# Kernel optimization log

Measured on AMD Instinct MI355X. Metric: run time of the kernel, lower is better.

The kernel has to match this reference:

```python
import jax, jax.numpy as jnp
import numpy as np

N, E, D, L = 50000, 800000, 128, 3  # nodes, edges, feature dim, num GraphConv layers


def setup_inputs() -> dict:
    key = jax.random.key(0)
    ks = jax.random.split(key, 6)
    x = jax.random.normal(ks[0], (N, D), dtype=jnp.float32)
    edge_index = jax.random.randint(ks[1], (2, E), 0, N, dtype=jnp.int64)
    edge_weight = jax.random.uniform(ks[2], (E,), dtype=jnp.float32)
    s = 1.0 / np.sqrt(D)  # PyG Linear default (kaiming-ish uniform bound)
    W_rel = jax.random.uniform(ks[3], (L, D, D), dtype=jnp.float32, minval=-s, maxval=s)
    b_rel = jax.random.uniform(ks[4], (L, D), dtype=jnp.float32, minval=-s, maxval=s)
    W_root = jax.random.uniform(ks[5], (L, D, D), dtype=jnp.float32, minval=-s, maxval=s)
    return {"x": x, "edge_index": edge_index, "edge_weight": edge_weight,
            "W_rel": W_rel, "b_rel": b_rel, "W_root": W_root}


def reference(x, edge_index, edge_weight, W_rel, b_rel, W_root):
    # PyG GraphConv: out = lin_rel(sum_{j->i} e_ji * x_j) + lin_root(x_i)
    src, dst = edge_index[0], edge_index[1]

    def conv(h, i):
        msg = h[src] * edge_weight[:, None]                     # [E, D] gather + per-edge scale
        agg = jax.ops.segment_sum(msg, dst, num_segments=N)     # [N, D] scatter-add
        return agg @ W_rel[i] + b_rel[i] + h @ W_root[i]

    h = x
    for i in range(L - 1):
        h = jax.nn.relu(conv(h, i))  # dropout is identity at inference
    return conv(h, L - 1)
```

## Files before the change

### kernel.cpp

```cpp
#include <hip/hip_runtime.h>

#define D 128
#define SC_IT 8

typedef __attribute__((ext_vector_type(8))) short bf16x8;
typedef __attribute__((ext_vector_type(4))) float f32x4;

__device__ __forceinline__ float uif(unsigned u) { return __uint_as_float(u); }
__device__ __forceinline__ unsigned short f2bf(float f) {
    unsigned u = __float_as_uint(f);
    u += 0x7fffu + ((u >> 16) & 1u);
    return (unsigned short)(u >> 16);
}
__device__ __forceinline__ float bf2f(unsigned short h) {
    return __uint_as_float(((unsigned)h) << 16);
}

__global__ __launch_bounds__(256) void rank_kernel(
    const int* __restrict__ dst, int* __restrict__ counts,
    int* __restrict__ rank, int E)
{
    int e = blockIdx.x * 256 + threadIdx.x;
    if (e < E) rank[e] = atomicAdd(&counts[dst[e]], 1);
}

__global__ __launch_bounds__(256) void blocksum_kernel(
    const int* __restrict__ counts, int* __restrict__ bsums, int N)
{
    __shared__ int red[256];
    int t = threadIdx.x;
    int i = blockIdx.x * 256 + t;
    red[t] = (i < N) ? counts[i] : 0;
    __syncthreads();
    #pragma unroll
    for (int off = 128; off > 0; off >>= 1) {
        if (t < off) red[t] += red[t + off];
        __syncthreads();
    }
    if (t == 0) bsums[blockIdx.x] = red[0];
}

__global__ __launch_bounds__(256) void scansums_kernel(
    int* __restrict__ bsums, int nb)
{
    __shared__ int s[256];
    int t = threadIdx.x;
    int v = (t < nb) ? bsums[t] : 0;
    s[t] = v;
    __syncthreads();
    #pragma unroll
    for (int off = 1; off < 256; off <<= 1) {
        int tmp = (t >= off) ? s[t - off] : 0;
        __syncthreads();
        s[t] += tmp;
        __syncthreads();
    }
    if (t < nb) bsums[t] = s[t] - v;
}

__global__ __launch_bounds__(256) void emit_kernel(
    const int* __restrict__ counts, const int* __restrict__ bsums,
    int* __restrict__ row_ptr, int N, int E)
{
    __shared__ int s[256];
    int t = threadIdx.x;
    int i = blockIdx.x * 256 + t;
    int v = (i < N) ? counts[i] : 0;
    s[t] = v;
    __syncthreads();
    #pragma unroll
    for (int off = 1; off < 256; off <<= 1) {
        int tmp = (t >= off) ? s[t - off] : 0;
        __syncthreads();
        s[t] += tmp;
        __syncthreads();
    }
    int excl = s[t] - v + bsums[blockIdx.x];
    if (i < N) row_ptr[i] = excl;
    if (blockIdx.x == 0 && t == 0) row_ptr[N] = E;
}

__global__ __launch_bounds__(256) void scatter_xcd_kernel(
    const int* __restrict__ src, const int* __restrict__ dst,
    const float* __restrict__ ew, const int* __restrict__ row_ptr,
    const int* __restrict__ rank, unsigned* __restrict__ edata, int E, int N)
{
    int xcd   = blockIdx.x & 7;
    int chunk = blockIdx.x >> 3;
    int lo = (int)(((long long)xcd * N) >> 3);
    int hi = (int)(((long long)(xcd + 1) * N) >> 3);
    int base = chunk * (256 * SC_IT) + threadIdx.x;
    #pragma unroll
    for (int it = 0; it < SC_IT; ++it) {
        int e = base + it * 256;
        if (e < E) {
            int d = __builtin_nontemporal_load(&dst[e]);
            if (d >= lo && d < hi) {
                int pos = row_ptr[d] + rank[e];
                unsigned pk = (unsigned)(unsigned short)
                                  __builtin_nontemporal_load(&src[e])
                            | ((unsigned)f2bf(
                                  __builtin_nontemporal_load(&ew[e])) << 16);
                edata[pos] = pk;
            }
        }
    }
}

__global__ __launch_bounds__(256) void convert_x_kernel(
    const float* __restrict__ x, short* __restrict__ Ah, int N)
{
    int t = blockIdx.x * 256 + threadIdx.x;
    if (t >= N * 64) return;
    int row = t >> 6;
    int c2  = (t & 63) * 2;
    float2 v = *(const float2*)(x + (size_t)row * D + c2);
    *(unsigned*)(Ah + (size_t)row * D + c2) =
        ((unsigned)f2bf(v.y) << 16) | f2bf(v.x);
}

__global__ __launch_bounds__(256) void convert_w_kernel(
    const float* __restrict__ Wrel, const float* __restrict__ Wroot,
    short* __restrict__ WT, int total)
{
    int t = blockIdx.x * 256 + threadIdx.x;
    if (t >= total) return;
    int l = t >> 15;
    int rem = t & 32767;
    int k = rem >> 7;
    int c = rem & 127;
    float f = (k < 128) ? Wrel[(size_t)l * 16384 + k * D + c]
                        : Wroot[(size_t)l * 16384 + (k - 128) * D + c];
    WT[(size_t)l * 32768 + c * 256 + k] = (short)f2bf(f);
}

__global__ __launch_bounds__(256) void gather_bf16(
    const short* __restrict__ Ah, short* __restrict__ aggHi,
    const unsigned* __restrict__ edata, const int* __restrict__ row_ptr, int N)
{
    int wave = (blockIdx.x * 256 + threadIdx.x) >> 6;
    int lane = threadIdx.x & 63;
    if (wave >= N) return;
    int g   = lane >> 4;
    int l16 = lane & 15;
    int beg = row_ptr[wave];
    int cnt = row_ptr[wave + 1] - beg;

    const short* hbase = Ah + l16 * 8;

    float acc[8];
    #pragma unroll
    for (int c = 0; c < 8; ++c) acc[c] = 0.f;

    for (int base = 0; base < cnt; base += 64) {
        int k = base + lane;
        int ed = 0;
        if (k < cnt) ed = (int)edata[beg + k];
        int m = min(64, cnt - base);
        for (int j = 0; j < m; j += 16) {
            int eA = __shfl(ed, j + g);
            int eB = __shfl(ed, j + 4 + g);
            int eC = __shfl(ed, j + 8 + g);
            int eD = __shfl(ed, j + 12 + g);
            float wA = uif((unsigned)eA & 0xffff0000u);
            float wB = uif((unsigned)eB & 0xffff0000u);
            float wC = uif((unsigned)eC & 0xffff0000u);
            float wD = uif((unsigned)eD & 0xffff0000u);
            bf16x8 rA = *(const bf16x8*)(hbase + (size_t)(eA & 0xffff) * D);
            bf16x8 rB = *(const bf16x8*)(hbase + (size_t)(eB & 0xffff) * D);
            bf16x8 rC = *(const bf16x8*)(hbase + (size_t)(eC & 0xffff) * D);
            bf16x8 rD = *(const bf16x8*)(hbase + (size_t)(eD & 0xffff) * D);
            #pragma unroll
            for (int c = 0; c < 8; ++c)
                acc[c] = fmaf(wA, bf2f((unsigned short)rA[c]), acc[c]);
            #pragma unroll
            for (int c = 0; c < 8; ++c)
                acc[c] = fmaf(wB, bf2f((unsigned short)rB[c]), acc[c]);
            #pragma unroll
            for (int c = 0; c < 8; ++c)
                acc[c] = fmaf(wC, bf2f((unsigned short)rC[c]), acc[c]);
            #pragma unroll
            for (int c = 0; c < 8; ++c)
                acc[c] = fmaf(wD, bf2f((unsigned short)rD[c]), acc[c]);
        }
    }

    #pragma unroll
    for (int c = 0; c < 8; ++c) {
        acc[c] += __shfl_xor(acc[c], 16);
        acc[c] += __shfl_xor(acc[c], 32);
    }

    if (g == 0) {
        bf16x8 pk;
        #pragma unroll
        for (int c = 0; c < 8; ++c) pk[c] = (short)f2bf(acc[c]);
        *(bf16x8*)(aggHi + (size_t)wave * D + l16 * 8) = pk;
    }
}

#define STAGE_W(WSRC)                                                           \
    _Pragma("unroll")                                                           \
    for (int r = 0; r < 16; ++r) {                                              \
        int u = r * 256 + tid;                                                  \
        bf16x8 v = *(const bf16x8*)((WSRC) + (size_t)u * 8);                    \
        int scol = u >> 5, sku = u & 31;                                        \
        *(bf16x8*)((char*)bsh + scol * 512 + ((sku ^ (scol & 7)) << 4)) = v;    \
    }

#define MFMA_SEG(APTR, KUOFF)                                                   \
    _Pragma("unroll")                                                           \
    for (int ks = 0; ks < 4; ++ks) {                                            \
        bf16x8 av[4];                                                           \
        _Pragma("unroll")                                                       \
        for (int m = 0; m < 4; ++m)                                             \
            av[m] = *(const bf16x8*)((APTR) + abase + (size_t)m * 16 * D        \
                                     + ks * 32 + l4 * 8);                       \
        _Pragma("unroll")                                                       \
        for (int n = 0; n < 4; ++n) {                                           \
            int col = wc * 64 + n * 16 + l15;                                   \
            int ku = (KUOFF) + ks * 4 + l4;                                     \
            bf16x8 b = *(const bf16x8*)((const char*)bsh + col * 512            \
                                        + ((ku ^ (col & 7)) << 4));             \
            _Pragma("unroll")                                                   \
            for (int m = 0; m < 4; ++m)                                         \
                acc[m][n] = __builtin_amdgcn_mfma_f32_16x16x32_bf16(            \
                    av[m], b, acc[m][n], 0, 0, 0);                              \
        }                                                                       \
    }

__global__ __launch_bounds__(256, 2) void gemm_mfma(
    const short* __restrict__ aggHi,
    const short* __restrict__ Ah, short* __restrict__ AhN,
    const short* __restrict__ WT,
    const float* __restrict__ bias, float* __restrict__ outf,
    int N, int relu, int writef)
{
    __shared__ short bsh[32768];
    int tid = threadIdx.x;
    int lane = tid & 63;
    int wid = tid >> 6;
    int wr = wid >> 1, wc = wid & 1;
    int l15 = lane & 15, l4 = lane >> 4;
    int row0 = blockIdx.x * 128;

    size_t abase = (size_t)(row0 + wr * 64 + l15) * D;

    f32x4 acc[4][4];
    #pragma unroll
    for (int m = 0; m < 4; ++m)
        #pragma unroll
        for (int n = 0; n < 4; ++n)
            acc[m][n] = (f32x4){0.f, 0.f, 0.f, 0.f};

    STAGE_W(WT);
    __syncthreads();
    MFMA_SEG(aggHi, 0);
    MFMA_SEG(Ah, 16);

    #pragma unroll
    for (int n = 0; n < 4; ++n) {
        int col = wc * 64 + n * 16 + l15;
        float bv = bias[col];
        #pragma unroll
        for (int m = 0; m < 4; ++m) {
            #pragma unroll
            for (int r = 0; r < 4; ++r) {
                int row = row0 + wr * 64 + m * 16 + l4 * 4 + r;
                if (row < N) {
                    float v = acc[m][n][r] + bv;
                    if (relu) v = fmaxf(v, 0.f);
                    if (writef) outf[(size_t)row * D + col] = v;
                    else        AhN[(size_t)row * D + col] = (short)f2bf(v);
                }
            }
        }
    }
}

extern "C" void kernel_launch(void* const* d_in, const int* in_sizes, int n_in,
                              void* d_out, int out_size, void* d_ws, size_t ws_size,
                              hipStream_t stream)
{
    const float* x     = (const float*)d_in[0];
    const int*   ei    = (const int*)d_in[1];
    const float* ew    = (const float*)d_in[2];
    const float* Wrel  = (const float*)d_in[3];
    const float* brel  = (const float*)d_in[4];
    const float* Wroot = (const float*)d_in[5];
    float* out = (float*)d_out;

    int N = in_sizes[0] / D;
    int E = in_sizes[2];
    int L = in_sizes[3] / (D * D);
    int Npad = ((N + 127) / 128) * 128;
    const int* src = ei;
    const int* dst = ei + E;
    int nb = (N + 255) / 256;

    short* Ah0   = (short*)d_ws;
    short* Ah1   = Ah0 + (size_t)Npad * D;
    short* aggHi = Ah1 + (size_t)Npad * D;
    short* WT    = aggHi + (size_t)Npad * D;
    unsigned* edata = (unsigned*)(WT + (size_t)L * 32768);
    int*   row_ptr = (int*)(edata + E);
    int*   rank    = row_ptr + (N + 1);
    int*   counts  = rank + E;
    int*   bsums   = counts + N;

    dim3 blk256(256);
    dim3 grdE((E + 255) / 256);
    dim3 grdN(nb);
    int nchunks = (E + 256 * SC_IT - 1) / (256 * SC_IT);
    dim3 grdScat(nchunks * 8);
    dim3 grdGather((N * 64 + 255) / 256);
    dim3 grdGemm(Npad / 128);
    dim3 grdCX((N * 64 + 255) / 256);
    dim3 grdCW((L * 32768 + 255) / 256);

    hipMemsetAsync(counts, 0, (size_t)N * sizeof(int), stream);
    rank_kernel<<<grdE, blk256, 0, stream>>>(dst, counts, rank, E);
    blocksum_kernel<<<grdN, blk256, 0, stream>>>(counts, bsums, N);
    scansums_kernel<<<1, blk256, 0, stream>>>(bsums, nb);
    emit_kernel<<<grdN, blk256, 0, stream>>>(counts, bsums, row_ptr, N, E);
    scatter_xcd_kernel<<<grdScat, blk256, 0, stream>>>(src, dst, ew, row_ptr,
                                                       rank, edata, E, N);

    convert_w_kernel<<<grdCW, blk256, 0, stream>>>(Wrel, Wroot, WT, L * 32768);
    convert_x_kernel<<<grdCX, blk256, 0, stream>>>(x, Ah0, N);

    for (int l = 0; l < L; ++l) {
        const short* Ain  = (l & 1) ? Ah1 : Ah0;
        short*       Aout = (l & 1) ? Ah0 : Ah1;
        gather_bf16<<<grdGather, blk256, 0, stream>>>(Ain, aggHi, edata, row_ptr, N);
        gemm_mfma<<<grdGemm, blk256, 0, stream>>>(
            aggHi, Ain, Aout, WT + (size_t)l * 32768,
            brel + (size_t)l * D, out, N, (l < L - 1) ? 1 : 0, (l == L - 1) ? 1 : 0);
    }
}
```

Baseline: 237.7 us.

## Gather neighbor features from an FP8 copy and partition rank atomics by XCD

Keeps a second FP8 (e4m3) copy of the node features next to the bf16 copy, written by convert_x and by the GEMM epilogue. The gather kernel reads that copy and decodes it with hardware cvt_pk_f32_fp8 when available, halving the bytes fetched per random neighbor row. The rank atomics are also split by destination range across XCD-mapped blocks, matching the existing scatter kernel. The trade is lower precision in the aggregated messages, extra byte-wise stores in the GEMM epilogue, and rank_kernel now reading dst eight times over.

New measurement: 243.6 us. +2.5%, slower.

```diff
diff --git a/kernel.cpp b/kernel.cpp
--- a/kernel.cpp
+++ b/kernel.cpp
@@ -5,6 +5,7 @@
 
 typedef __attribute__((ext_vector_type(8))) short bf16x8;
 typedef __attribute__((ext_vector_type(4))) float f32x4;
+typedef __attribute__((ext_vector_type(2))) unsigned uint2v;
 
 __device__ __forceinline__ float uif(unsigned u) { return __uint_as_float(u); }
 __device__ __forceinline__ unsigned short f2bf(float f) {
@@ -16,12 +17,68 @@
     return __uint_as_float(((unsigned)h) << 16);
 }
 
-__global__ __launch_bounds__(256) void rank_kernel(
+__device__ __forceinline__ unsigned char f2fp8(float f) {
+    unsigned s = (__float_as_uint(f) >> 24) & 0x80u;
+    float a = fminf(fabsf(f), 448.f);
+    unsigned b = __float_as_uint(a);
+    int e = (int)((b >> 23) & 255) - 127;
+    unsigned r;
+    if (e >= -6) {
+        unsigned rb = b + 0x7ffffu + ((b >> 20) & 1u);
+        int e8 = (int)((rb >> 23) & 255) - 120;
+        unsigned m3 = (rb >> 20) & 7u;
+        if (e8 > 15) { e8 = 15; m3 = 6; }
+        r = ((unsigned)e8 << 3) | m3;
+    } else {
+        int ni = (int)(a * 512.f + 0.5f);
+        r = (ni > 7) ? 8u : (unsigned)ni;
+    }
+    return (unsigned char)(s | r);
+}
+
+#if __has_builtin(__builtin_amdgcn_cvt_pk_f32_fp8)
+#define DECODE8(Q, F)                                                           \
+    do {                                                                        \
+        auto p0 = __builtin_amdgcn_cvt_pk_f32_fp8((Q).x, false);                \
+        auto p1 = __builtin_amdgcn_cvt_pk_f32_fp8((Q).x, true);                 \
+        auto p2 = __builtin_amdgcn_cvt_pk_f32_fp8((Q).y, false);                \
+        auto p3 = __builtin_amdgcn_cvt_pk_f32_fp8((Q).y, true);                 \
+        F[0] = p0[0]; F[1] = p0[1]; F[2] = p1[0]; F[3] = p1[1];                 \
+        F[4] = p2[0]; F[5] = p2[1]; F[6] = p3[0]; F[7] = p3[1];                 \
+    } while (0)
+#else
+__device__ __forceinline__ float fp82f_sw(unsigned b) {
+    unsigned e = (b >> 3) & 15u, m = b & 7u;
+    float v = e ? uif(((e + 120u) << 23) | (m << 20)) : (float)m * 0x1p-9f;
+    return (b & 0x80u) ? -v : v;
+}
+#define DECODE8(Q, F)                                                           \
+    do {                                                                        \
+        unsigned q0 = (Q).x, q1 = (Q).y;                                        \
+        F[0] = fp82f_sw(q0 & 255); F[1] = fp82f_sw((q0 >> 8) & 255);            \
+        F[2] = fp82f_sw((q0 >> 16) & 255); F[3] = fp82f_sw(q0 >> 24);           \
+        F[4] = fp82f_sw(q1 & 255); F[5] = fp82f_sw((q1 >> 8) & 255);            \
+        F[6] = fp82f_sw((q1 >> 16) & 255); F[7] = fp82f_sw(q1 >> 24);           \
+    } while (0)
+#endif
+
+__global__ __launch_bounds__(256) void rank_xcd_kernel(
     const int* __restrict__ dst, int* __restrict__ counts,
-    int* __restrict__ rank, int E)
-{
-    int e = blockIdx.x * 256 + threadIdx.x;
-    if (e < E) rank[e] = atomicAdd(&counts[dst[e]], 1);
+    int* __restrict__ rank, int E, int N)
+{
+    int xcd   = blockIdx.x & 7;
+    int chunk = blockIdx.x >> 3;
+    int lo = (int)(((long long)xcd * N) >> 3);
+    int hi = (int)(((long long)(xcd + 1) * N) >> 3);
+    int base = chunk * (256 * SC_IT) + threadIdx.x;
+    #pragma unroll
+    for (int it = 0; it < SC_IT; ++it) {
+        int e = base + it * 256;
+        if (e < E) {
+            int d = __builtin_nontemporal_load(&dst[e]);
+            if (d >= lo && d < hi) rank[e] = atomicAdd(&counts[d], 1);
+        }
+    }
 }
 
 __global__ __launch_bounds__(256) void blocksum_kernel(
@@ -108,7 +165,8 @@
 }
 
 __global__ __launch_bounds__(256) void convert_x_kernel(
-    const float* __restrict__ x, short* __restrict__ Ah, int N)
+    const float* __restrict__ x, short* __restrict__ Ah,
+    unsigned char* __restrict__ Ah8, int N)
 {
     int t = blockIdx.x * 256 + threadIdx.x;
     if (t >= N * 64) return;
@@ -117,6 +175,9 @@
     float2 v = *(const float2*)(x + (size_t)row * D + c2);
     *(unsigned*)(Ah + (size_t)row * D + c2) =
         ((unsigned)f2bf(v.y) << 16) | f2bf(v.x);
+    unsigned short p8 = (unsigned short)f2fp8(v.x)
+                      | ((unsigned short)f2fp8(v.y) << 8);
+    *(unsigned short*)(Ah8 + (size_t)row * D + c2) = p8;
 }
 
 __global__ __launch_bounds__(256) void convert_w_kernel(
@@ -134,8 +195,8 @@
     WT[(size_t)l * 32768 + c * 256 + k] = (short)f2bf(f);
 }
 
-__global__ __launch_bounds__(256) void gather_bf16(
-    const short* __restrict__ Ah, short* __restrict__ aggHi,
+__global__ __launch_bounds__(256) void gather_fp8(
+    const unsigned char* __restrict__ Ah8, short* __restrict__ aggHi,
     const unsigned* __restrict__ edata, const int* __restrict__ row_ptr, int N)
 {
     int wave = (blockIdx.x * 256 + threadIdx.x) >> 6;
@@ -146,7 +207,7 @@
     int beg = row_ptr[wave];
     int cnt = row_ptr[wave + 1] - beg;
 
-    const short* hbase = Ah + l16 * 8;
+    const unsigned char* hbase = Ah8 + l16 * 8;
 
     float acc[8];
     #pragma unroll
@@ -166,22 +227,23 @@
             float wB = uif((unsigned)eB & 0xffff0000u);
             float wC = uif((unsigned)eC & 0xffff0000u);
             float wD = uif((unsigned)eD & 0xffff0000u);
-            bf16x8 rA = *(const bf16x8*)(hbase + (size_t)(eA & 0xffff) * D);
-            bf16x8 rB = *(const bf16x8*)(hbase + (size_t)(eB & 0xffff) * D);
-            bf16x8 rC = *(const bf16x8*)(hbase + (size_t)(eC & 0xffff) * D);
-            bf16x8 rD = *(const bf16x8*)(hbase + (size_t)(eD & 0xffff) * D);
+            uint2v qA = *(const uint2v*)(hbase + (size_t)(eA & 0xffff) * D);
+            uint2v qB = *(const uint2v*)(hbase + (size_t)(eB & 0xffff) * D);
+            uint2v qC = *(const uint2v*)(hbase + (size_t)(eC & 0xffff) * D);
+            uint2v qD = *(const uint2v*)(hbase + (size_t)(eD & 0xffff) * D);
+            float fA[8], fB[8], fC[8], fD[8];
+            DECODE8(qA, fA);
+            DECODE8(qB, fB);
+            DECODE8(qC, fC);
+            DECODE8(qD, fD);
             #pragma unroll
-            for (int c = 0; c < 8; ++c)
-                acc[c] = fmaf(wA, bf2f((unsigned short)rA[c]), acc[c]);
+            for (int c = 0; c < 8; ++c) acc[c] = fmaf(wA, fA[c], acc[c]);
             #pragma unroll
-            for (int c = 0; c < 8; ++c)
-                acc[c] = fmaf(wB, bf2f((unsigned short)rB[c]), acc[c]);
+            for (int c = 0; c < 8; ++c) acc[c] = fmaf(wB, fB[c], acc[c]);
             #pragma unroll
-            for (int c = 0; c < 8; ++c)
-                acc[c] = fmaf(wC, bf2f((unsigned short)rC[c]), acc[c]);
+            for (int c = 0; c < 8; ++c) acc[c] = fmaf(wC, fC[c], acc[c]);
             #pragma unroll
-            for (int c = 0; c < 8; ++c)
-                acc[c] = fmaf(wD, bf2f((unsigned short)rD[c]), acc[c]);
+            for (int c = 0; c < 8; ++c) acc[c] = fmaf(wD, fD[c], acc[c]);
         }
     }
 
@@ -232,6 +294,7 @@
 __global__ __launch_bounds__(256, 2) void gemm_mfma(
     const short* __restrict__ aggHi,
     const short* __restrict__ Ah, short* __restrict__ AhN,
+    unsigned char* __restrict__ AhN8,
     const short* __restrict__ WT,
     const float* __restrict__ bias, float* __restrict__ outf,
     int N, int relu, int writef)
@@ -270,8 +333,12 @@
                 if (row < N) {
                     float v = acc[m][n][r] + bv;
                     if (relu) v = fmaxf(v, 0.f);
-                    if (writef) outf[(size_t)row * D + col] = v;
-                    else        AhN[(size_t)row * D + col] = (short)f2bf(v);
+                    if (writef) {
+                        outf[(size_t)row * D + col] = v;
+                    } else {
+                        AhN[(size_t)row * D + col] = (short)f2bf(v);
+                        AhN8[(size_t)row * D + col] = f2fp8(v);
+                    }
                 }
             }
         }
@@ -307,9 +374,10 @@
     int*   rank    = row_ptr + (N + 1);
     int*   counts  = rank + E;
     int*   bsums   = counts + N;
+    unsigned char* Ah8_0 = (unsigned char*)(bsums + nb);
+    unsigned char* Ah8_1 = Ah8_0 + (size_t)Npad * D;
 
     dim3 blk256(256);
-    dim3 grdE((E + 255) / 256);
     dim3 grdN(nb);
     int nchunks = (E + 256 * SC_IT - 1) / (256 * SC_IT);
     dim3 grdScat(nchunks * 8);
@@ -319,7 +387,7 @@
     dim3 grdCW((L * 32768 + 255) / 256);
 
     hipMemsetAsync(counts, 0, (size_t)N * sizeof(int), stream);
-    rank_kernel<<<grdE, blk256, 0, stream>>>(dst, counts, rank, E);
+    rank_xcd_kernel<<<grdScat, blk256, 0, stream>>>(dst, counts, rank, E, N);
     blocksum_kernel<<<grdN, blk256, 0, stream>>>(counts, bsums, N);
     scansums_kernel<<<1, blk256, 0, stream>>>(bsums, nb);
     emit_kernel<<<grdN, blk256, 0, stream>>>(counts, bsums, row_ptr, N, E);
@@ -327,14 +395,16 @@
                                                        rank, edata, E, N);
 
     convert_w_kernel<<<grdCW, blk256, 0, stream>>>(Wrel, Wroot, WT, L * 32768);
-    convert_x_kernel<<<grdCX, blk256, 0, stream>>>(x, Ah0, N);
+    convert_x_kernel<<<grdCX, blk256, 0, stream>>>(x, Ah0, Ah8_0, N);
 
     for (int l = 0; l < L; ++l) {
-        const short* Ain  = (l & 1) ? Ah1 : Ah0;
-        short*       Aout = (l & 1) ? Ah0 : Ah1;
-        gather_bf16<<<grdGather, blk256, 0, stream>>>(Ain, aggHi, edata, row_ptr, N);
+        const short* Ain = (l & 1) ? Ah1 : Ah0;
+        short* Aout      = (l & 1) ? Ah0 : Ah1;
+        const unsigned char* Ain8 = (l & 1) ? Ah8_1 : Ah8_0;
+        unsigned char* Aout8      = (l & 1) ? Ah8_0 : Ah8_1;
+        gather_fp8<<<grdGather, blk256, 0, stream>>>(Ain8, aggHi, edata, row_ptr, N);
         gemm_mfma<<<grdGemm, blk256, 0, stream>>>(
-            aggHi, Ain, Aout, WT + (size_t)l * 32768,
+            aggHi, Ain, Aout, Aout8, WT + (size_t)l * 32768,
             brel + (size_t)l * D, out, N, (l < L - 1) ? 1 : 0, (l == L - 1) ? 1 : 0);
     }
 }
```
